# Kernel tuning notes

Measured on AMD Instinct MI355X. Metric: run time of the kernel, lower is better.

Reference implementation:

```python
import jax, jax.numpy as jnp
import numpy as np


def setup_inputs() -> dict:
    key = jax.random.key(0)
    T, B, D, H = 512, 64, 512, 512
    k0, k1, k2, k3 = jax.random.split(key, 4)
    x = jax.random.normal(k0, (T, B, D), dtype=jnp.float32)
    # packed-sequence lengths, descending (as PackedSequence requires), at least T//2
    lengths = jnp.sort(jax.random.randint(k1, (B,), T // 2, T + 1))[::-1].astype(jnp.int64)
    s = 1.0 / np.sqrt(H)
    # gates stacked in order (i, f, c, o): same math as 8 separate per-gate linears
    Wx = jax.random.normal(k2, (4 * H, D), dtype=jnp.float32) * s
    Wh = jax.random.normal(k3, (4 * H, H), dtype=jnp.float32) * s
    # reset_parameters(): b_i = b_c = b_o = 0, b_f = 1
    b = jnp.concatenate([jnp.zeros(H), jnp.ones(H), jnp.zeros(2 * H)]).astype(jnp.float32)
    return {"x": x, "lengths": lengths, "Wx": Wx, "Wh": Wh, "b": b}


def reference(x, lengths, Wx, Wh, b):
    T, B, D = x.shape
    H = Wh.shape[1]
    # input projections for all timesteps at once (one big GEMM)
    xg = jnp.einsum('tbd,gd->tbg', x, Wx) + b  # [T, B, 4H]
    # validity mask per (t, b): packed recurrence only updates active rows
    mask = (jnp.arange(T)[:, None] < lengths[None, :])[..., None]  # [T, B, 1]

    def step(carry, inp):
        h, c = carry
        xg_t, m = inp
        g = xg_t + h @ Wh.T  # [B, 4H]
        i, f, cc, o = jnp.split(g, 4, axis=-1)
        i = jax.nn.sigmoid(i)
        f = jax.nn.sigmoid(f)
        o = jax.nn.sigmoid(o)
        c_t = f * c + i * jnp.tanh(cc)
        h_t = o * jnp.tanh(c_t)
        c_new = jnp.where(m, c_t, c)
        h_new = jnp.where(m, h_t, h)
        out_t = jnp.where(m, h_new, jnp.zeros((), x.dtype))
        return (h_new, c_new), out_t

    h0 = jnp.zeros((B, H), dtype=x.dtype)
    (h_T, c_T), out = jax.lax.scan(step, (h0, h0), (xg, mask))
    return out  # padded equivalent of the PackedSequence output, [T, B, H]
```

## Files before the change

### kernel.cpp

```cpp
#include <hip/hip_runtime.h>
#include <stdint.h>


#define TT 512
#define BB 64
#define DD 512
#define HH 512
#define NTHR 512
#define NWG2 128
#define GR2 16
#define NWG4 256
#define GR4 8

typedef short short8 __attribute__((ext_vector_type(8)));
typedef float f32x4 __attribute__((ext_vector_type(4)));

__device__ __forceinline__ uint16_t bf16_rne(float f) {
  uint32_t u = __float_as_uint(f);
  u += 0x7fffu + ((u >> 16) & 1u);
  return (uint16_t)(u >> 16);
}

__device__ __forceinline__ void split2(float f, uint16_t &hi, uint16_t &lo) {
  uint16_t h = bf16_rne(f);
  hi = h;
  lo = bf16_rne(f - __uint_as_float(((uint32_t)h) << 16));
}

__device__ __forceinline__ float sigf(float v) { return 1.0f / (1.0f + __expf(-v)); }
__device__ __forceinline__ float tanh_(float v) {
  return 1.0f - 2.0f / (__expf(2.0f * v) + 1.0f);
}

__global__ void build_frags(const float* __restrict__ W, uint32_t* __restrict__ frag) {
  const int tid = blockIdx.x * 256 + threadIdx.x;
  const int lane = tid & 63;
  const int ks = (tid >> 6) & 15;
  const int nblk = tid >> 10;
  const int col = nblk * 16 + (lane & 15);
  const int k0 = ks * 32 + ((lane >> 4) << 3);
  const float* src = W + (size_t)col * 512 + k0;
  float4 a = *(const float4*)(src);
  float4 b = *(const float4*)(src + 4);
  float v[8] = {a.x, a.y, a.z, a.w, b.x, b.y, b.z, b.w};
  uint32_t hw[4], lw[4];
#pragma unroll
  for (int j = 0; j < 4; ++j) {
    uint16_t h0, l0, h1, l1;
    split2(v[2 * j], h0, l0);
    split2(v[2 * j + 1], h1, l1);
    hw[j] = (uint32_t)h0 | ((uint32_t)h1 << 16);
    lw[j] = (uint32_t)l0 | ((uint32_t)l1 << 16);
  }
  uint4* dst = (uint4*)(frag + (size_t)tid * 8);
  dst[0] = make_uint4(hw[0], hw[1], hw[2], hw[3]);
  dst[1] = make_uint4(lw[0], lw[1], lw[2], lw[3]);
}

__global__ __launch_bounds__(NTHR, 1) void xg_gemm(
    const float* __restrict__ x, const float* __restrict__ bias,
    const uint32_t* __restrict__ fragWx, float* __restrict__ xg) {
  const int t = blockIdx.x;
  const int tid = threadIdx.x;
  const int lane = tid & 63;
  const int wave = tid >> 6;
  const int gate = wave & 3;
  const int jsub = wave >> 2;

  __shared__ uint16_t AH[64 * 512];
  __shared__ uint16_t AL[64 * 512];

#pragma unroll
  for (int i = 0; i < 16; ++i) {
    const int flat4 = i * 2048 + tid * 4;
    const int row = flat4 >> 9;
    const int col = flat4 & 511;
    float4 v = *(const float4*)(x + ((size_t)t * BB + row) * DD + col);
    uint16_t h0, l0, h1, l1, h2, l2, h3, l3;
    split2(v.x, h0, l0);
    split2(v.y, h1, l1);
    split2(v.z, h2, l2);
    split2(v.w, h3, l3);
    const int off = row * 1024 + ((col * 2) ^ ((row & 7) << 4));
    *(uint2*)((char*)AH + off) =
        make_uint2((uint32_t)h0 | ((uint32_t)h1 << 16), (uint32_t)h2 | ((uint32_t)h3 << 16));
    *(uint2*)((char*)AL + off) =
        make_uint2((uint32_t)l0 | ((uint32_t)l1 << 16), (uint32_t)l2 | ((uint32_t)l3 << 16));
  }
  __syncthreads();

  const int achk = (lane >> 4) << 4;
  const int axr = (lane & 7) << 4;

  for (int jp = 0; jp < 16; ++jp) {
    const int jblk = jp * 2 + jsub;
    const int nblk = gate * 32 + jblk;
    short8 bh[16], bl[16];
#pragma unroll
    for (int ks = 0; ks < 16; ++ks) {
      const size_t idx = ((size_t)(nblk * 16 + ks) * 64 + lane) * 8;
      bh[ks] = __builtin_bit_cast(short8, *(const uint4*)(fragWx + idx));
      bl[ks] = __builtin_bit_cast(short8, *(const uint4*)(fragWx + idx + 4));
    }
    const int colg = (nblk << 4) + (lane & 15);
    const float bv = bias[colg];
    for (int m = 0; m < 4; ++m) {
      const char* rowH = (const char*)AH + (m * 16 + (lane & 15)) * 1024;
      const char* rowL = (const char*)AL + (m * 16 + (lane & 15)) * 1024;
      f32x4 hh = {0.f, 0.f, 0.f, 0.f}, lh = {0.f, 0.f, 0.f, 0.f}, hl = {0.f, 0.f, 0.f, 0.f};
#pragma unroll
      for (int ks = 0; ks < 16; ++ks) {
        const int off = (ks * 64 + achk) ^ axr;
        short8 ah = *(const short8*)(rowH + off);
        short8 al = *(const short8*)(rowL + off);
        hh = __builtin_amdgcn_mfma_f32_16x16x32_bf16(ah, bh[ks], hh, 0, 0, 0);
        lh = __builtin_amdgcn_mfma_f32_16x16x32_bf16(al, bh[ks], lh, 0, 0, 0);
        hl = __builtin_amdgcn_mfma_f32_16x16x32_bf16(ah, bl[ks], hl, 0, 0, 0);
      }
      const int r0 = m * 16 + ((lane >> 4) << 2);
#pragma unroll
      for (int i = 0; i < 4; ++i)
        xg[((size_t)t * BB + r0 + i) * 2048 + colg] = hh[i] + lh[i] + hl[i] + bv;
    }
  }
}

__global__ __launch_bounds__(NTHR, 2) void lstm2(
    const int* __restrict__ len, const uint32_t* __restrict__ fragWh,
    const float* __restrict__ xg, uint32_t* __restrict__ h_pair,
    float* __restrict__ out) {
  const int tid = threadIdx.x;
  const int lane = tid & 63;
  const int wave = tid >> 6;
  const int gp = wave >> 1;
  const int kh = wave & 1;
  const int group = blockIdx.x & 3;
  const int jblk = blockIdx.x >> 2;
  const int b0 = group * GR2;
  const int j0 = jblk << 4;
  uint32_t* hbase = h_pair + (size_t)group * 2 * (GR2 * HH);

  __shared__ uint16_t AH[GR2 * 512];
  __shared__ uint16_t AL[GR2 * 512];
  __shared__ float ex[8][GR2][16];
  __shared__ float c_st[GR2][16];
  __shared__ float h_st[GR2][16];
  __shared__ int len_l[GR2];

  if (tid < GR2 * 16) {
    c_st[tid >> 4][tid & 15] = 0.0f;
    h_st[tid >> 4][tid & 15] = 0.0f;
  }
  if (tid < GR2) len_l[tid] = len[b0 + tid];

  short8 bhh[8], bhl[8];
  {
    const int nblk = gp * 32 + jblk;
#pragma unroll
    for (int ksl = 0; ksl < 8; ++ksl) {
      const size_t idx = ((size_t)(nblk * 16 + kh * 8 + ksl) * 64 + lane) * 8;
      bhh[ksl] = __builtin_bit_cast(short8, *(const uint4*)(fragWh + idx));
      bhl[ksl] = __builtin_bit_cast(short8, *(const uint4*)(fragWh + idx + 4));
    }
  }

  const int arow = lane & 15;
  const int achk = (lane >> 4) << 4;
  const int axr = (arow & 7) << 4;
  const char* rowH = (const char*)AH + arow * 1024;
  const char* rowL = (const char*)AL + arow * 1024;

  const int brow = tid >> 4;
  const int jc = tid & 15;

  float xc0 = 0.f, xc1 = 0.f, xc2 = 0.f, xc3 = 0.f;
  float xn0 = 0.f, xn1 = 0.f, xn2 = 0.f, xn3 = 0.f;
  if (tid < 256) {
    const size_t xb = ((size_t)b0 + brow) * 2048 + j0 + jc;
    xc0 = xg[xb];
    xc1 = xg[xb + 512];
    xc2 = xg[xb + 1024];
    xc3 = xg[xb + 1536];
  }

  for (int t = 0; t < TT; ++t) {
    const int rbuf = t & 1;
    const int wbuf = rbuf ^ 1;

    if (tid < 256) {
      const int tn = (t + 1 < TT) ? t + 1 : t;
      const size_t xb = ((size_t)tn * BB + b0 + brow) * 2048 + j0 + jc;
      xn0 = xg[xb];
      xn1 = xg[xb + 512];
      xn2 = xg[xb + 1024];
      xn3 = xg[xb + 1536];
    }

    f32x4 hh = {0.f, 0.f, 0.f, 0.f}, lh = {0.f, 0.f, 0.f, 0.f}, hl = {0.f, 0.f, 0.f, 0.f};

    if (t > 0) {
      const uint32_t tagp = (((uint32_t)(t - 1)) >> 1) & 3u;
      const uint32_t EXd = ((tagp & 1u) << 14) | ((tagp >> 1) << 30);
      const uint64_t EX2 = ((uint64_t)EXd << 32) | EXd;
      const uint64_t MK2 = 0x4000400040004000ull;
      const unsigned long long* pb =
          (const unsigned long long*)(hbase + (size_t)rbuf * (GR2 * HH)) +
          (size_t)tid * 8;
      uint64_t w[8];
      for (;;) {
#pragma unroll
        for (int q = 0; q < 8; ++q)
          w[q] = __hip_atomic_load(pb + q, __ATOMIC_RELAXED, __HIP_MEMORY_SCOPE_AGENT);
        uint64_t bad = 0;
#pragma unroll
        for (int q = 0; q < 8; ++q) bad |= (w[q] ^ EX2);
        if ((bad & MK2) == 0ull) break;
      }

      {
        const uint32_t CM = ~0x40004000u;
        uint32_t d[16];
#pragma unroll
        for (int q = 0; q < 8; ++q) {
          d[2 * q] = (uint32_t)w[q] & CM;
          d[2 * q + 1] = (uint32_t)(w[q] >> 32) & CM;
        }
        uint32_t hw[8], lw[8];
#pragma unroll
        for (int j = 0; j < 8; ++j) {
          hw[j] = (d[2 * j] & 0xFFFFu) | (d[2 * j + 1] << 16);
          lw[j] = (d[2 * j] >> 16) | (d[2 * j + 1] & 0xFFFF0000u);
        }
        const int rrow = tid >> 5;
        const int colb = (tid & 31) * 32;
        const int base = rrow * 1024;
        const int swz = (rrow & 7) << 4;
        *(uint4*)((char*)AH + base + (colb ^ swz)) = make_uint4(hw[0], hw[1], hw[2], hw[3]);
        *(uint4*)((char*)AH + base + ((colb + 16) ^ swz)) = make_uint4(hw[4], hw[5], hw[6], hw[7]);
        *(uint4*)((char*)AL + base + (colb ^ swz)) = make_uint4(lw[0], lw[1], lw[2], lw[3]);
        *(uint4*)((char*)AL + base + ((colb + 16) ^ swz)) = make_uint4(lw[4], lw[5], lw[6], lw[7]);
      }
    }
    __syncthreads();

    if (t > 0) {
#pragma unroll
      for (int ksl = 0; ksl < 8; ++ksl) {
        const int off = ((kh * 8 + ksl) * 64 + achk) ^ axr;
        short8 ah = *(const short8*)(rowH + off);
        short8 al = *(const short8*)(rowL + off);
        hh = __builtin_amdgcn_mfma_f32_16x16x32_bf16(ah, bhh[ksl], hh, 0, 0, 0);
        lh = __builtin_amdgcn_mfma_f32_16x16x32_bf16(al, bhh[ksl], lh, 0, 0, 0);
        hl = __builtin_amdgcn_mfma_f32_16x16x32_bf16(ah, bhl[ksl], hl, 0, 0, 0);
      }
    }

    {
      const int crow = (lane >> 4) << 2;
      const int ccol = lane & 15;
#pragma unroll
      for (int r = 0; r < 4; ++r) ex[wave][crow + r][ccol] = hh[r] + lh[r] + hl[r];
    }
    __syncthreads();

    if (tid < 256) {
      const float p0 = ex[0][brow][jc] + ex[1][brow][jc] + xc0;
      const float p1 = ex[2][brow][jc] + ex[3][brow][jc] + xc1;
      const float p2 = ex[4][brow][jc] + ex[5][brow][jc] + xc2;
      const float p3 = ex[6][brow][jc] + ex[7][brow][jc] + xc3;
      const float ig = sigf(p0);
      const float fg = sigf(p1);
      const float cc = tanh_(p2);
      const float og = sigf(p3);
      const float co = c_st[brow][jc];
      const float ct = fg * co + ig * cc;
      const float ht = og * tanh_(ct);
      const bool m = (t < len_l[brow]);
      const float cn = m ? ct : co;
      const float hn = m ? ht : h_st[brow][jc];
      c_st[brow][jc] = cn;
      h_st[brow][jc] = hn;
      out[((size_t)t * BB + b0 + brow) * HH + j0 + jc] = m ? ht : 0.0f;
      uint16_t ph, pl;
      split2(hn, ph, pl);
      const uint32_t tagw = (((uint32_t)t) >> 1) & 3u;
      const uint32_t TB = ((tagw & 1u) << 14) | ((tagw >> 1) << 30);
      __hip_atomic_store(hbase + (size_t)wbuf * (GR2 * HH) + brow * HH + j0 + jc,
                         ((uint32_t)ph | ((uint32_t)pl << 16)) | TB,
                         __ATOMIC_RELAXED, __HIP_MEMORY_SCOPE_AGENT);
      xc0 = xn0;
      xc1 = xn1;
      xc2 = xn2;
      xc3 = xn3;
    }
  }
}

#define LOAD_XP(tt)                                                            \
  _Pragma("unroll") for (int i = 0; i < 2; ++i) {                              \
    const int flat4 = i * 2048 + tid * 4;                                      \
    const int row = flat4 >> 9;                                                \
    const int col = flat4 & 511;                                               \
    xp[i] = *(const float4*)(x + ((size_t)(tt) * BB + b0 + row) * DD + col);   \
  }

#define STAGE_XP()                                                             \
  _Pragma("unroll") for (int i = 0; i < 2; ++i) {                              \
    const int flat4 = i * 2048 + tid * 4;                                      \
    const int row = flat4 >> 9;                                                \
    const int col = flat4 & 511;                                               \
    uint16_t h0, l0, h1, l1, h2, l2, h3, l3;                                   \
    split2(xp[i].x, h0, l0);                                                   \
    split2(xp[i].y, h1, l1);                                                   \
    split2(xp[i].z, h2, l2);                                                   \
    split2(xp[i].w, h3, l3);                                                   \
    const uint32_t hw0 = (uint32_t)h0 | ((uint32_t)h1 << 16);                  \
    const uint32_t hw1 = (uint32_t)h2 | ((uint32_t)h3 << 16);                  \
    const uint32_t lw0 = (uint32_t)l0 | ((uint32_t)l1 << 16);                  \
    const uint32_t lw1 = (uint32_t)l2 | ((uint32_t)l3 << 16);                  \
    const int off = row * 1024 + ((col * 2) ^ (row << 4));                     \
    *(uint2*)((char*)AH + off) = make_uint2(hw0, hw1);                         \
    *(uint2*)((char*)AL + off) = make_uint2(lw0, lw1);                         \
  }

#define X_MFMA()                                                               \
  hh = (f32x4){0.f, 0.f, 0.f, 0.f};                                           \
  lh = (f32x4){0.f, 0.f, 0.f, 0.f};                                           \
  hl = (f32x4){0.f, 0.f, 0.f, 0.f};                                           \
  _Pragma("unroll") for (int ksl = 0; ksl < 8; ++ksl) {                        \
    const int off = ((kh * 8 + ksl) * 64 + achk) ^ axr;                        \
    short8 ah = *(const short8*)(rowH + off);                                  \
    short8 al = *(const short8*)(rowL + off);                                  \
    hh = __builtin_amdgcn_mfma_f32_16x16x32_bf16(ah, bxh[ksl], hh, 0, 0, 0);   \
    lh = __builtin_amdgcn_mfma_f32_16x16x32_bf16(al, bxh[ksl], lh, 0, 0, 0);   \
    hl = __builtin_amdgcn_mfma_f32_16x16x32_bf16(ah, bxl[ksl], hl, 0, 0, 0);   \
  }

__global__ __launch_bounds__(NTHR, 2) void lstm_r4(
    const float* __restrict__ x, const int* __restrict__ len,
    const float* __restrict__ bias, const uint32_t* __restrict__ fragWx,
    const uint32_t* __restrict__ fragWh, uint32_t* __restrict__ h_pair,
    float* __restrict__ out) {
  const int tid = threadIdx.x;
  const int lane = tid & 63;
  const int wave = tid >> 6;
  const int gp = wave >> 1;
  const int kh = wave & 1;
  const int group = blockIdx.x & 7;
  const int jblk = blockIdx.x >> 3;
  const int b0 = group * GR4;
  const int j0 = jblk << 4;
  uint32_t* hbase = h_pair + (size_t)group * 2 * (GR4 * HH);

  __shared__ uint16_t AH[GR4 * 512];
  __shared__ uint16_t AL[GR4 * 512];
  __shared__ float ex[8][GR4][16];
  __shared__ float c_st[GR4][16];
  __shared__ float h_st[GR4][16];
  __shared__ float bias_l[4][16];
  __shared__ int len_l[GR4];

  if (tid < GR4 * 16) {
    c_st[tid >> 4][tid & 15] = 0.0f;
    h_st[tid >> 4][tid & 15] = 0.0f;
  }
  if (tid < 64) bias_l[tid >> 4][tid & 15] = bias[(size_t)(tid >> 4) * HH + j0 + (tid & 15)];
  if (tid < GR4) len_l[tid] = len[b0 + tid];

  short8 bxh[8], bxl[8], bhh[8], bhl[8];
  {
    const int nblk = gp * 32 + jblk;
#pragma unroll
    for (int ksl = 0; ksl < 8; ++ksl) {
      const size_t idx = ((size_t)(nblk * 16 + kh * 8 + ksl) * 64 + lane) * 8;
      bxh[ksl] = __builtin_bit_cast(short8, *(const uint4*)(fragWx + idx));
      bxl[ksl] = __builtin_bit_cast(short8, *(const uint4*)(fragWx + idx + 4));
      bhh[ksl] = __builtin_bit_cast(short8, *(const uint4*)(fragWh + idx));
      bhl[ksl] = __builtin_bit_cast(short8, *(const uint4*)(fragWh + idx + 4));
    }
  }

  const int arow = lane & 7;
  const int achk = (lane >> 4) << 4;
  const int axr = arow << 4;
  const char* rowH = (const char*)AH + arow * 1024;
  const char* rowL = (const char*)AL + arow * 1024;

  f32x4 hh = {0.f, 0.f, 0.f, 0.f}, lh = {0.f, 0.f, 0.f, 0.f}, hl = {0.f, 0.f, 0.f, 0.f};
  float4 xp[2];

  LOAD_XP(0);
  __syncthreads();
  STAGE_XP();
  __syncthreads();
  X_MFMA();
  LOAD_XP(1);

  for (int t = 0; t < TT; ++t) {
    const int rbuf = t & 1;
    const int wbuf = rbuf ^ 1;

    if (t > 0) {
      const uint32_t tagp = (((uint32_t)(t - 1)) >> 1) & 3u;
      const uint32_t EXd = ((tagp & 1u) << 14) | ((tagp >> 1) << 30);
      const uint64_t EX2 = ((uint64_t)EXd << 32) | EXd;
      const uint64_t MK2 = 0x4000400040004000ull;
      const unsigned long long* pb =
          (const unsigned long long*)(hbase + (size_t)rbuf * (GR4 * HH)) +
          (size_t)tid * 4;
      uint64_t w0, w1, w2, w3;
      for (;;) {
        w0 = __hip_atomic_load(pb + 0, __ATOMIC_RELAXED, __HIP_MEMORY_SCOPE_AGENT);
        w1 = __hip_atomic_load(pb + 1, __ATOMIC_RELAXED, __HIP_MEMORY_SCOPE_AGENT);
        w2 = __hip_atomic_load(pb + 2, __ATOMIC_RELAXED, __HIP_MEMORY_SCOPE_AGENT);
        w3 = __hip_atomic_load(pb + 3, __ATOMIC_RELAXED, __HIP_MEMORY_SCOPE_AGENT);
        const uint64_t bad =
            (((w0 ^ EX2) | (w1 ^ EX2) | (w2 ^ EX2) | (w3 ^ EX2)) & MK2);
        if (bad == 0ull) break;
      }
      __syncthreads();

      {
        const uint32_t CM = ~0x40004000u;
        uint32_t d0 = (uint32_t)w0 & CM, d1 = (uint32_t)(w0 >> 32) & CM;
        uint32_t d2 = (uint32_t)w1 & CM, d3 = (uint32_t)(w1 >> 32) & CM;
        uint32_t d4 = (uint32_t)w2 & CM, d5 = (uint32_t)(w2 >> 32) & CM;
        uint32_t d6 = (uint32_t)w3 & CM, d7 = (uint32_t)(w3 >> 32) & CM;
        const uint32_t hi0 = (d0 & 0xFFFFu) | (d1 << 16);
        const uint32_t lo0 = (d0 >> 16) | (d1 & 0xFFFF0000u);
        const uint32_t hi1 = (d2 & 0xFFFFu) | (d3 << 16);
        const uint32_t lo1 = (d2 >> 16) | (d3 & 0xFFFF0000u);
        const uint32_t hi2 = (d4 & 0xFFFFu) | (d5 << 16);
        const uint32_t lo2 = (d4 >> 16) | (d5 & 0xFFFF0000u);
        const uint32_t hi3 = (d6 & 0xFFFFu) | (d7 << 16);
        const uint32_t lo3 = (d6 >> 16) | (d7 & 0xFFFF0000u);
        const int woff = wave * 1024 + ((lane * 16) ^ (wave << 4));
        *(uint4*)((char*)AH + woff) = make_uint4(hi0, hi1, hi2, hi3);
        *(uint4*)((char*)AL + woff) = make_uint4(lo0, lo1, lo2, lo3);
      }
      __syncthreads();

#pragma unroll
      for (int ksl = 0; ksl < 8; ++ksl) {
        const int off = ((kh * 8 + ksl) * 64 + achk) ^ axr;
        short8 ah = *(const short8*)(rowH + off);
        short8 al = *(const short8*)(rowL + off);
        hh = __builtin_amdgcn_mfma_f32_16x16x32_bf16(ah, bhh[ksl], hh, 0, 0, 0);
        lh = __builtin_amdgcn_mfma_f32_16x16x32_bf16(al, bhh[ksl], lh, 0, 0, 0);
        hl = __builtin_amdgcn_mfma_f32_16x16x32_bf16(ah, bhl[ksl], hl, 0, 0, 0);
      }
    }

    {
      const int crow = (lane >> 4) << 2;
      const int ccol = lane & 15;
      if (crow < GR4) {
#pragma unroll
        for (int r = 0; r < 4; ++r) ex[wave][crow + r][ccol] = hh[r] + lh[r] + hl[r];
      }
    }
    __syncthreads();

    if (tid < GR4 * 16) {
      const int brow = tid >> 4;
      const int jc = tid & 15;
      const float p0 = ex[0][brow][jc] + ex[1][brow][jc] + bias_l[0][jc];
      const float p1 = ex[2][brow][jc] + ex[3][brow][jc] + bias_l[1][jc];
      const float p2 = ex[4][brow][jc] + ex[5][brow][jc] + bias_l[2][jc];
      const float p3 = ex[6][brow][jc] + ex[7][brow][jc] + bias_l[3][jc];
      const float ig = sigf(p0);
      const float fg = sigf(p1);
      const float cc = tanh_(p2);
      const float og = sigf(p3);
      const float co = c_st[brow][jc];
      const float ct = fg * co + ig * cc;
      const float ht = og * tanh_(ct);
      const bool m = (t < len_l[brow]);
      const float cn = m ? ct : co;
      const float hn = m ? ht : h_st[brow][jc];
      c_st[brow][jc] = cn;
      h_st[brow][jc] = hn;
      out[((size_t)t * BB + b0 + brow) * HH + j0 + jc] = m ? ht : 0.0f;
      uint16_t ph, pl;
      split2(hn, ph, pl);
      const uint32_t tagw = (((uint32_t)t) >> 1) & 3u;
      const uint32_t TB = ((tagw & 1u) << 14) | ((tagw >> 1) << 30);
      const uint32_t hv = ((uint32_t)ph | ((uint32_t)pl << 16)) | TB;
      __hip_atomic_store(hbase + (size_t)wbuf * (GR4 * HH) + brow * HH + j0 + jc,
                         hv, __ATOMIC_RELAXED, __HIP_MEMORY_SCOPE_AGENT);
    }

    if (t + 1 < TT) {
      STAGE_XP();
      __syncthreads();
      X_MFMA();
      LOAD_XP(min(t + 2, TT - 1));
    }
  }
}
#undef LOAD_XP
#undef STAGE_XP
#undef X_MFMA

extern "C" void kernel_launch(void* const* d_in, const int* in_sizes, int n_in,
                              void* d_out, int out_size, void* d_ws, size_t ws_size,
                              hipStream_t stream) {
  const float* x = (const float*)d_in[0];
  const int* len = (const int*)d_in[1];
  const float* Wx = (const float*)d_in[2];
  const float* Wh = (const float*)d_in[3];
  const float* bias = (const float*)d_in[4];
  float* out = (float*)d_out;

  const size_t FRAG_DW = (size_t)128 * 16 * 64 * 8;
  const size_t HP_DW = 65536;
  const size_t XG_DW = (size_t)TT * BB * 2048;
  uint32_t* fragWx = (uint32_t*)d_ws;
  uint32_t* fragWh = fragWx + FRAG_DW;
  uint32_t* h_pair = fragWh + FRAG_DW;
  float* xg = (float*)(h_pair + HP_DW);
  const size_t need = (2 * FRAG_DW + HP_DW + XG_DW) * 4;

  hipMemsetAsync(h_pair, 0xFF, HP_DW * 4, stream);

  build_frags<<<dim3(512), dim3(256), 0, stream>>>(Wx, fragWx);
  build_frags<<<dim3(512), dim3(256), 0, stream>>>(Wh, fragWh);

  if (ws_size >= need) {
    xg_gemm<<<dim3(TT), dim3(NTHR), 0, stream>>>(x, bias, fragWx, xg);
    void* args[] = {(void*)&len, (void*)&fragWh, (void*)&xg, (void*)&h_pair,
                    (void*)&out};
    hipLaunchCooperativeKernel((void*)lstm2, dim3(NWG2), dim3(NTHR), args, 0, stream);
  } else {
    void* args[] = {(void*)&x,      (void*)&len,    (void*)&bias, (void*)&fragWx,
                    (void*)&fragWh, (void*)&h_pair, (void*)&out};
    hipLaunchCooperativeKernel((void*)lstm_r4, dim3(NWG4), dim3(NTHR), args, 0, stream);
  }
}
```

Baseline: 1.439 ms.

## Fuse input projection into recurrent kernel via producer workgroups feeding a ring buffer

Removes the separate xg GEMM kernel and its large global xg buffer. The cooperative launch now has twice as many workgroups: half run the recurrence, and the other half compute each timestep's input projection plus bias just ahead of it. Projections pass through a 4-slot tagged ring buffer packed as hi/lo bf16, with a per-pair counter for flow control. The goal is to overlap the input GEMM with the serial recurrence and avoid the xg round trip through memory. In exchange, projections are scaled and clamped to ±64 before packing, which could lose accuracy on large inputs, and correctness now depends on all 256 workgroups being co-resident.

```diff
diff --git a/kernel.cpp b/kernel.cpp
--- a/kernel.cpp
+++ b/kernel.cpp
@@ -7,8 +7,9 @@
 #define DD 512
 #define HH 512
 #define NTHR 512
-#define NWG2 128
-#define GR2 16
+#define NWG 256
+#define NPAIR 128
+#define GR 16
 #define NWG4 256
 #define GR4 8
 
@@ -57,112 +58,34 @@
   dst[1] = make_uint4(lw[0], lw[1], lw[2], lw[3]);
 }
 
-__global__ __launch_bounds__(NTHR, 1) void xg_gemm(
-    const float* __restrict__ x, const float* __restrict__ bias,
-    const uint32_t* __restrict__ fragWx, float* __restrict__ xg) {
-  const int t = blockIdx.x;
-  const int tid = threadIdx.x;
-  const int lane = tid & 63;
-  const int wave = tid >> 6;
-  const int gate = wave & 3;
-  const int jsub = wave >> 2;
-
-  __shared__ uint16_t AH[64 * 512];
-  __shared__ uint16_t AL[64 * 512];
-
-#pragma unroll
-  for (int i = 0; i < 16; ++i) {
-    const int flat4 = i * 2048 + tid * 4;
-    const int row = flat4 >> 9;
-    const int col = flat4 & 511;
-    float4 v = *(const float4*)(x + ((size_t)t * BB + row) * DD + col);
-    uint16_t h0, l0, h1, l1, h2, l2, h3, l3;
-    split2(v.x, h0, l0);
-    split2(v.y, h1, l1);
-    split2(v.z, h2, l2);
-    split2(v.w, h3, l3);
-    const int off = row * 1024 + ((col * 2) ^ ((row & 7) << 4));
-    *(uint2*)((char*)AH + off) =
-        make_uint2((uint32_t)h0 | ((uint32_t)h1 << 16), (uint32_t)h2 | ((uint32_t)h3 << 16));
-    *(uint2*)((char*)AL + off) =
-        make_uint2((uint32_t)l0 | ((uint32_t)l1 << 16), (uint32_t)l2 | ((uint32_t)l3 << 16));
-  }
-  __syncthreads();
-
-  const int achk = (lane >> 4) << 4;
-  const int axr = (lane & 7) << 4;
-
-  for (int jp = 0; jp < 16; ++jp) {
-    const int jblk = jp * 2 + jsub;
-    const int nblk = gate * 32 + jblk;
-    short8 bh[16], bl[16];
-#pragma unroll
-    for (int ks = 0; ks < 16; ++ks) {
-      const size_t idx = ((size_t)(nblk * 16 + ks) * 64 + lane) * 8;
-      bh[ks] = __builtin_bit_cast(short8, *(const uint4*)(fragWx + idx));
-      bl[ks] = __builtin_bit_cast(short8, *(const uint4*)(fragWx + idx + 4));
-    }
-    const int colg = (nblk << 4) + (lane & 15);
-    const float bv = bias[colg];
-    for (int m = 0; m < 4; ++m) {
-      const char* rowH = (const char*)AH + (m * 16 + (lane & 15)) * 1024;
-      const char* rowL = (const char*)AL + (m * 16 + (lane & 15)) * 1024;
-      f32x4 hh = {0.f, 0.f, 0.f, 0.f}, lh = {0.f, 0.f, 0.f, 0.f}, hl = {0.f, 0.f, 0.f, 0.f};
-#pragma unroll
-      for (int ks = 0; ks < 16; ++ks) {
-        const int off = (ks * 64 + achk) ^ axr;
-        short8 ah = *(const short8*)(rowH + off);
-        short8 al = *(const short8*)(rowL + off);
-        hh = __builtin_amdgcn_mfma_f32_16x16x32_bf16(ah, bh[ks], hh, 0, 0, 0);
-        lh = __builtin_amdgcn_mfma_f32_16x16x32_bf16(al, bh[ks], lh, 0, 0, 0);
-        hl = __builtin_amdgcn_mfma_f32_16x16x32_bf16(ah, bl[ks], hl, 0, 0, 0);
-      }
-      const int r0 = m * 16 + ((lane >> 4) << 2);
-#pragma unroll
-      for (int i = 0; i < 4; ++i)
-        xg[((size_t)t * BB + r0 + i) * 2048 + colg] = hh[i] + lh[i] + hl[i] + bv;
-    }
-  }
-}
-
-__global__ __launch_bounds__(NTHR, 2) void lstm2(
-    const int* __restrict__ len, const uint32_t* __restrict__ fragWh,
-    const float* __restrict__ xg, uint32_t* __restrict__ h_pair,
+__global__ __launch_bounds__(NTHR, 2) void lstm3(
+    const float* __restrict__ x, const int* __restrict__ len,
+    const float* __restrict__ bias, const uint32_t* __restrict__ fragWx,
+    const uint32_t* __restrict__ fragWh, uint32_t* __restrict__ h_pair,
+    uint32_t* __restrict__ xacc, uint32_t* __restrict__ cnts,
     float* __restrict__ out) {
   const int tid = threadIdx.x;
   const int lane = tid & 63;
   const int wave = tid >> 6;
   const int gp = wave >> 1;
   const int kh = wave & 1;
-  const int group = blockIdx.x & 3;
-  const int jblk = blockIdx.x >> 2;
-  const int b0 = group * GR2;
+  const bool isH = blockIdx.x < NPAIR;
+  const int pid = isH ? blockIdx.x : blockIdx.x - NPAIR;
+  const int group = pid & 3;
+  const int jblk = pid >> 2;
+  const int b0 = group * GR;
   const int j0 = jblk << 4;
-  uint32_t* hbase = h_pair + (size_t)group * 2 * (GR2 * HH);
-
-  __shared__ uint16_t AH[GR2 * 512];
-  __shared__ uint16_t AL[GR2 * 512];
-  __shared__ float ex[8][GR2][16];
-  __shared__ float c_st[GR2][16];
-  __shared__ float h_st[GR2][16];
-  __shared__ int len_l[GR2];
-
-  if (tid < GR2 * 16) {
-    c_st[tid >> 4][tid & 15] = 0.0f;
-    h_st[tid >> 4][tid & 15] = 0.0f;
-  }
-  if (tid < GR2) len_l[tid] = len[b0 + tid];
-
-  short8 bhh[8], bhl[8];
-  {
-    const int nblk = gp * 32 + jblk;
-#pragma unroll
-    for (int ksl = 0; ksl < 8; ++ksl) {
-      const size_t idx = ((size_t)(nblk * 16 + kh * 8 + ksl) * 64 + lane) * 8;
-      bhh[ksl] = __builtin_bit_cast(short8, *(const uint4*)(fragWh + idx));
-      bhl[ksl] = __builtin_bit_cast(short8, *(const uint4*)(fragWh + idx + 4));
-    }
-  }
+  uint32_t* hbase = h_pair + (size_t)group * 2 * (GR * HH);
+  unsigned long long* xb64 = (unsigned long long*)(xacc + (size_t)pid * 4096);
+
+  __shared__ uint16_t AH[GR * 512];
+  __shared__ uint16_t AL[GR * 512];
+  __shared__ float ex[8][GR][16];
+  __shared__ float xex[GR][64];
+  __shared__ float c_st[GR][16];
+  __shared__ float h_st[GR][16];
+  __shared__ float bias_l[4][16];
+  __shared__ int len_l[GR];
 
   const int arow = lane & 15;
   const int achk = (lane >> 4) << 4;
@@ -170,128 +93,236 @@
   const char* rowH = (const char*)AH + arow * 1024;
   const char* rowL = (const char*)AL + arow * 1024;
 
-  const int brow = tid >> 4;
-  const int jc = tid & 15;
-
-  float xc0 = 0.f, xc1 = 0.f, xc2 = 0.f, xc3 = 0.f;
-  float xn0 = 0.f, xn1 = 0.f, xn2 = 0.f, xn3 = 0.f;
-  if (tid < 256) {
-    const size_t xb = ((size_t)b0 + brow) * 2048 + j0 + jc;
-    xc0 = xg[xb];
-    xc1 = xg[xb + 512];
-    xc2 = xg[xb + 1024];
-    xc3 = xg[xb + 1536];
-  }
-
-  for (int t = 0; t < TT; ++t) {
-    const int rbuf = t & 1;
-    const int wbuf = rbuf ^ 1;
-
+  const uint64_t MK2 = 0x4000400040004000ull;
+  const uint32_t CM = ~0x40004000u;
+
+  if (isH) {
     if (tid < 256) {
-      const int tn = (t + 1 < TT) ? t + 1 : t;
-      const size_t xb = ((size_t)tn * BB + b0 + brow) * 2048 + j0 + jc;
-      xn0 = xg[xb];
-      xn1 = xg[xb + 512];
-      xn2 = xg[xb + 1024];
-      xn3 = xg[xb + 1536];
-    }
-
-    f32x4 hh = {0.f, 0.f, 0.f, 0.f}, lh = {0.f, 0.f, 0.f, 0.f}, hl = {0.f, 0.f, 0.f, 0.f};
-
-    if (t > 0) {
-      const uint32_t tagp = (((uint32_t)(t - 1)) >> 1) & 3u;
-      const uint32_t EXd = ((tagp & 1u) << 14) | ((tagp >> 1) << 30);
+      c_st[tid >> 4][tid & 15] = 0.0f;
+      h_st[tid >> 4][tid & 15] = 0.0f;
+    }
+    if (tid < GR) len_l[tid] = len[b0 + tid];
+
+    short8 bhh[8], bhl[8];
+    {
+      const int nblk = gp * 32 + jblk;
+#pragma unroll
+      for (int ksl = 0; ksl < 8; ++ksl) {
+        const size_t idx = ((size_t)(nblk * 16 + kh * 8 + ksl) * 64 + lane) * 8;
+        bhh[ksl] = __builtin_bit_cast(short8, *(const uint4*)(fragWh + idx));
+        bhl[ksl] = __builtin_bit_cast(short8, *(const uint4*)(fragWh + idx + 4));
+      }
+    }
+
+    const int prow = tid >> 5;
+    const int pc0 = tid & 31;
+    const int brow = tid >> 4;
+    const int jc = tid & 15;
+
+    for (int t = 0; t < TT; ++t) {
+      const int rbuf = t & 1;
+      const int wbuf = rbuf ^ 1;
+
+      const uint32_t tagh = (((uint32_t)(t - 1)) >> 1) & 3u;
+      const uint32_t EHd = ((tagh & 1u) << 14) | ((tagh >> 1) << 30);
+      const uint64_t EH2 = ((uint64_t)EHd << 32) | EHd;
+      const uint32_t tagx = (((uint32_t)t) >> 1) & 3u;
+      const uint32_t EXd = ((tagx & 1u) << 14) | ((tagx >> 1) << 30);
       const uint64_t EX2 = ((uint64_t)EXd << 32) | EXd;
-      const uint64_t MK2 = 0x4000400040004000ull;
-      const unsigned long long* pb =
-          (const unsigned long long*)(hbase + (size_t)rbuf * (GR2 * HH)) +
-          (size_t)tid * 8;
-      uint64_t w[8];
-      for (;;) {
-#pragma unroll
-        for (int q = 0; q < 8; ++q)
-          w[q] = __hip_atomic_load(pb + q, __ATOMIC_RELAXED, __HIP_MEMORY_SCOPE_AGENT);
-        uint64_t bad = 0;
-#pragma unroll
-        for (int q = 0; q < 8; ++q) bad |= (w[q] ^ EX2);
-        if ((bad & MK2) == 0ull) break;
-      }
-
+
+      const unsigned long long* hb64 =
+          (const unsigned long long*)(hbase + (size_t)rbuf * (GR * HH));
+      const unsigned long long* hp0 = hb64 + prow * 256 + pc0 * 4;
+      const unsigned long long* hp1 = hp0 + 128;
+      const unsigned long long* xp = xb64 + (size_t)(t & 3) * 512 + tid;
+
+      uint64_t w0, w1, w2, w3, w4, w5, w6, w7, wx;
+      if (t > 0) {
+        for (;;) {
+          w0 = __hip_atomic_load(hp0 + 0, __ATOMIC_RELAXED, __HIP_MEMORY_SCOPE_AGENT);
+          w1 = __hip_atomic_load(hp0 + 1, __ATOMIC_RELAXED, __HIP_MEMORY_SCOPE_AGENT);
+          w2 = __hip_atomic_load(hp0 + 2, __ATOMIC_RELAXED, __HIP_MEMORY_SCOPE_AGENT);
+          w3 = __hip_atomic_load(hp0 + 3, __ATOMIC_RELAXED, __HIP_MEMORY_SCOPE_AGENT);
+          w4 = __hip_atomic_load(hp1 + 0, __ATOMIC_RELAXED, __HIP_MEMORY_SCOPE_AGENT);
+          w5 = __hip_atomic_load(hp1 + 1, __ATOMIC_RELAXED, __HIP_MEMORY_SCOPE_AGENT);
+          w6 = __hip_atomic_load(hp1 + 2, __ATOMIC_RELAXED, __HIP_MEMORY_SCOPE_AGENT);
+          w7 = __hip_atomic_load(hp1 + 3, __ATOMIC_RELAXED, __HIP_MEMORY_SCOPE_AGENT);
+          wx = __hip_atomic_load(xp, __ATOMIC_RELAXED, __HIP_MEMORY_SCOPE_AGENT);
+          const uint64_t bad = (((w0 ^ EH2) | (w1 ^ EH2) | (w2 ^ EH2) | (w3 ^ EH2) |
+                                (w4 ^ EH2) | (w5 ^ EH2) | (w6 ^ EH2) | (w7 ^ EH2) |
+                                (wx ^ EX2)) & MK2);
+          if (bad == 0ull) break;
+        }
+      } else {
+        for (;;) {
+          wx = __hip_atomic_load(xp, __ATOMIC_RELAXED, __HIP_MEMORY_SCOPE_AGENT);
+          if (((wx ^ EX2) & MK2) == 0ull) break;
+        }
+      }
+
+      if (t > 0) {
+        const int base = prow * 1024;
+        const int swz = (prow & 7) << 4;
+        uint32_t d0, d1, d2, d3, d4, d5, d6, d7;
+#define UNPK(A, B, C, D, OFF)                                                  \
+        d0 = (uint32_t)(A) & CM; d1 = (uint32_t)((A) >> 32) & CM;              \
+        d2 = (uint32_t)(B) & CM; d3 = (uint32_t)((B) >> 32) & CM;              \
+        d4 = (uint32_t)(C) & CM; d5 = (uint32_t)((C) >> 32) & CM;              \
+        d6 = (uint32_t)(D) & CM; d7 = (uint32_t)((D) >> 32) & CM;              \
+        *(uint4*)((char*)AH + base + ((OFF) ^ swz)) =                          \
+            make_uint4((d0 & 0xFFFFu) | (d1 << 16), (d2 & 0xFFFFu) | (d3 << 16), \
+                       (d4 & 0xFFFFu) | (d5 << 16), (d6 & 0xFFFFu) | (d7 << 16)); \
+        *(uint4*)((char*)AL + base + ((OFF) ^ swz)) =                          \
+            make_uint4((d0 >> 16) | (d1 & 0xFFFF0000u), (d2 >> 16) | (d3 & 0xFFFF0000u), \
+                       (d4 >> 16) | (d5 & 0xFFFF0000u), (d6 >> 16) | (d7 & 0xFFFF0000u));
+        UNPK(w0, w1, w2, w3, pc0 * 16);
+        UNPK(w4, w5, w6, w7, pc0 * 16 + 512);
+#undef UNPK
+      }
       {
-        const uint32_t CM = ~0x40004000u;
-        uint32_t d[16];
-#pragma unroll
-        for (int q = 0; q < 8; ++q) {
-          d[2 * q] = (uint32_t)w[q] & CM;
-          d[2 * q + 1] = (uint32_t)(w[q] >> 32) & CM;
+        const uint32_t da = (uint32_t)wx & CM;
+        const uint32_t db = (uint32_t)(wx >> 32) & CM;
+        const int f0 = 2 * tid;
+        xex[f0 >> 6][f0 & 63] =
+            32.0f * (__uint_as_float(da << 16) + __uint_as_float(da & 0xFFFF0000u));
+        xex[f0 >> 6][(f0 & 63) + 1] =
+            32.0f * (__uint_as_float(db << 16) + __uint_as_float(db & 0xFFFF0000u));
+      }
+      __syncthreads();
+
+      f32x4 hh = {0.f, 0.f, 0.f, 0.f}, lh = {0.f, 0.f, 0.f, 0.f}, hl = {0.f, 0.f, 0.f, 0.f};
+      if (t > 0) {
+#pragma unroll
+        for (int ksl = 0; ksl < 8; ++ksl) {
+          const int off = ((kh * 8 + ksl) * 64 + achk) ^ axr;
+          short8 ah = *(const short8*)(rowH + off);
+          short8 al = *(const short8*)(rowL + off);
+          hh = __builtin_amdgcn_mfma_f32_16x16x32_bf16(ah, bhh[ksl], hh, 0, 0, 0);
+          lh = __builtin_amdgcn_mfma_f32_16x16x32_bf16(al, bhh[ksl], lh, 0, 0, 0);
+          hl = __builtin_amdgcn_mfma_f32_16x16x32_bf16(ah, bhl[ksl], hl, 0, 0, 0);
         }
-        uint32_t hw[8], lw[8];
-#pragma unroll
-        for (int j = 0; j < 8; ++j) {
-          hw[j] = (d[2 * j] & 0xFFFFu) | (d[2 * j + 1] << 16);
-          lw[j] = (d[2 * j] >> 16) | (d[2 * j + 1] & 0xFFFF0000u);
+      }
+      {
+        const int crow = (lane >> 4) << 2;
+        const int ccol = lane & 15;
+#pragma unroll
+        for (int r = 0; r < 4; ++r) ex[wave][crow + r][ccol] = hh[r] + lh[r] + hl[r];
+      }
+      __syncthreads();
+
+      if (tid < 256) {
+        const float p0 = ex[0][brow][jc] + ex[1][brow][jc] + xex[brow][jc];
+        const float p1 = ex[2][brow][jc] + ex[3][brow][jc] + xex[brow][16 + jc];
+        const float p2 = ex[4][brow][jc] + ex[5][brow][jc] + xex[brow][32 + jc];
+        const float p3 = ex[6][brow][jc] + ex[7][brow][jc] + xex[brow][48 + jc];
+        const float ig = sigf(p0);
+        const float fg = sigf(p1);
+        const float cc = tanh_(p2);
+        const float og = sigf(p3);
+        const float co = c_st[brow][jc];
+        const float ct = fg * co + ig * cc;
+        const float ht = og * tanh_(ct);
+        const bool m = (t < len_l[brow]);
+        const float cn = m ? ct : co;
+        const float hn = m ? ht : h_st[brow][jc];
+        c_st[brow][jc] = cn;
+        h_st[brow][jc] = hn;
+        out[((size_t)t * BB + b0 + brow) * HH + j0 + jc] = m ? ht : 0.0f;
+        uint16_t ph, pl;
+        split2(hn, ph, pl);
+        const uint32_t tagw = (((uint32_t)t) >> 1) & 3u;
+        const uint32_t TB = ((tagw & 1u) << 14) | ((tagw >> 1) << 30);
+        __hip_atomic_store(hbase + (size_t)wbuf * (GR * HH) + brow * HH + j0 + jc,
+                           ((uint32_t)ph | ((uint32_t)pl << 16)) | TB,
+                           __ATOMIC_RELAXED, __HIP_MEMORY_SCOPE_AGENT);
+      }
+      if (tid == 0)
+        __hip_atomic_store(cnts + pid, (uint32_t)(t + 1), __ATOMIC_RELAXED,
+                           __HIP_MEMORY_SCOPE_AGENT);
+    }
+  } else {
+    if (tid < 64) bias_l[tid >> 4][tid & 15] = bias[(size_t)(tid >> 4) * HH + j0 + (tid & 15)];
+
+    short8 bxh[8], bxl[8];
+    {
+      const int nblk = gp * 32 + jblk;
+#pragma unroll
+      for (int ksl = 0; ksl < 8; ++ksl) {
+        const size_t idx = ((size_t)(nblk * 16 + kh * 8 + ksl) * 64 + lane) * 8;
+        bxh[ksl] = __builtin_bit_cast(short8, *(const uint4*)(fragWx + idx));
+        bxl[ksl] = __builtin_bit_cast(short8, *(const uint4*)(fragWx + idx + 4));
+      }
+    }
+
+    for (int t = 0; t < TT; ++t) {
+      if (t >= 4) {
+        for (;;) {
+          uint32_t c = __hip_atomic_load(cnts + pid, __ATOMIC_RELAXED,
+                                         __HIP_MEMORY_SCOPE_AGENT);
+          if ((int)c >= t - 3) break;
         }
-        const int rrow = tid >> 5;
-        const int colb = (tid & 31) * 32;
-        const int base = rrow * 1024;
-        const int swz = (rrow & 7) << 4;
-        *(uint4*)((char*)AH + base + (colb ^ swz)) = make_uint4(hw[0], hw[1], hw[2], hw[3]);
-        *(uint4*)((char*)AH + base + ((colb + 16) ^ swz)) = make_uint4(hw[4], hw[5], hw[6], hw[7]);
-        *(uint4*)((char*)AL + base + (colb ^ swz)) = make_uint4(lw[0], lw[1], lw[2], lw[3]);
-        *(uint4*)((char*)AL + base + ((colb + 16) ^ swz)) = make_uint4(lw[4], lw[5], lw[6], lw[7]);
-      }
-    }
-    __syncthreads();
-
-    if (t > 0) {
+      }
+#pragma unroll
+      for (int i = 0; i < 4; ++i) {
+        const int flat4 = i * 2048 + tid * 4;
+        const int row = flat4 >> 9;
+        const int col = flat4 & 511;
+        float4 v = *(const float4*)(x + ((size_t)t * BB + b0 + row) * DD + col);
+        uint16_t h0, l0, h1, l1, h2, l2, h3, l3;
+        split2(v.x, h0, l0);
+        split2(v.y, h1, l1);
+        split2(v.z, h2, l2);
+        split2(v.w, h3, l3);
+        const int off = row * 1024 + ((col * 2) ^ ((row & 7) << 4));
+        *(uint2*)((char*)AH + off) =
+            make_uint2((uint32_t)h0 | ((uint32_t)h1 << 16), (uint32_t)h2 | ((uint32_t)h3 << 16));
+        *(uint2*)((char*)AL + off) =
+            make_uint2((uint32_t)l0 | ((uint32_t)l1 << 16), (uint32_t)l2 | ((uint32_t)l3 << 16));
+      }
+      __syncthreads();
+
+      f32x4 hh = {0.f, 0.f, 0.f, 0.f}, lh = {0.f, 0.f, 0.f, 0.f}, hl = {0.f, 0.f, 0.f, 0.f};
 #pragma unroll
       for (int ksl = 0; ksl < 8; ++ksl) {
         const int off = ((kh * 8 + ksl) * 64 + achk) ^ axr;
         short8 ah = *(const short8*)(rowH + off);
         short8 al = *(const short8*)(rowL + off);
-        hh = __builtin_amdgcn_mfma_f32_16x16x32_bf16(ah, bhh[ksl], hh, 0, 0, 0);
-        lh = __builtin_amdgcn_mfma_f32_16x16x32_bf16(al, bhh[ksl], lh, 0, 0, 0);
-        hl = __builtin_amdgcn_mfma_f32_16x16x32_bf16(ah, bhl[ksl], hl, 0, 0, 0);
-      }
-    }
-
-    {
-      const int crow = (lane >> 4) << 2;
-      const int ccol = lane & 15;
-#pragma unroll
-      for (int r = 0; r < 4; ++r) ex[wave][crow + r][ccol] = hh[r] + lh[r] + hl[r];
-    }
-    __syncthreads();
-
-    if (tid < 256) {
-      const float p0 = ex[0][brow][jc] + ex[1][brow][jc] + xc0;
-      const float p1 = ex[2][brow][jc] + ex[3][brow][jc] + xc1;
-      const float p2 = ex[4][brow][jc] + ex[5][brow][jc] + xc2;
-      const float p3 = ex[6][brow][jc] + ex[7][brow][jc] + xc3;
-      const float ig = sigf(p0);
-      const float fg = sigf(p1);
-      const float cc = tanh_(p2);
-      const float og = sigf(p3);
-      const float co = c_st[brow][jc];
-      const float ct = fg * co + ig * cc;
-      const float ht = og * tanh_(ct);
-      const bool m = (t < len_l[brow]);
-      const float cn = m ? ct : co;
-      const float hn = m ? ht : h_st[brow][jc];
-      c_st[brow][jc] = cn;
-      h_st[brow][jc] = hn;
-      out[((size_t)t * BB + b0 + brow) * HH + j0 + jc] = m ? ht : 0.0f;
-      uint16_t ph, pl;
-      split2(hn, ph, pl);
-      const uint32_t tagw = (((uint32_t)t) >> 1) & 3u;
-      const uint32_t TB = ((tagw & 1u) << 14) | ((tagw >> 1) << 30);
-      __hip_atomic_store(hbase + (size_t)wbuf * (GR2 * HH) + brow * HH + j0 + jc,
-                         ((uint32_t)ph | ((uint32_t)pl << 16)) | TB,
-                         __ATOMIC_RELAXED, __HIP_MEMORY_SCOPE_AGENT);
-      xc0 = xn0;
-      xc1 = xn1;
-      xc2 = xn2;
-      xc3 = xn3;
+        hh = __builtin_amdgcn_mfma_f32_16x16x32_bf16(ah, bxh[ksl], hh, 0, 0, 0);
+        lh = __builtin_amdgcn_mfma_f32_16x16x32_bf16(al, bxh[ksl], lh, 0, 0, 0);
+        hl = __builtin_amdgcn_mfma_f32_16x16x32_bf16(ah, bxl[ksl], hl, 0, 0, 0);
+      }
+      {
+        const int crow = (lane >> 4) << 2;
+        const int ccol = lane & 15;
+#pragma unroll
+        for (int r = 0; r < 4; ++r) ex[wave][crow + r][ccol] = hh[r] + lh[r] + hl[r];
+      }
+      __syncthreads();
+
+      {
+        const int f0 = 2 * tid;
+        const int brow = f0 >> 6;
+        const int gc0 = f0 & 63;
+        const int gc1 = gc0 + 1;
+        const float p0 = ex[(gc0 >> 4) * 2][brow][gc0 & 15] +
+                         ex[(gc0 >> 4) * 2 + 1][brow][gc0 & 15] + bias_l[gc0 >> 4][gc0 & 15];
+        const float p1 = ex[(gc1 >> 4) * 2][brow][gc1 & 15] +
+                         ex[(gc1 >> 4) * 2 + 1][brow][gc1 & 15] + bias_l[gc1 >> 4][gc1 & 15];
+        const uint32_t tagw = (((uint32_t)t) >> 1) & 3u;
+        const uint32_t TB = ((tagw & 1u) << 14) | ((tagw >> 1) << 30);
+        float v0 = p0 * 0.03125f;
+        float v1 = p1 * 0.03125f;
+        v0 = fminf(fmaxf(v0, -1.9921875f), 1.9921875f);
+        v1 = fminf(fmaxf(v1, -1.9921875f), 1.9921875f);
+        uint16_t h0, l0, h1, l1;
+        split2(v0, h0, l0);
+        split2(v1, h1, l1);
+        const uint32_t da = ((uint32_t)h0 | ((uint32_t)l0 << 16)) | TB;
+        const uint32_t db = ((uint32_t)h1 | ((uint32_t)l1 << 16)) | TB;
+        __hip_atomic_store(xb64 + (size_t)(t & 3) * 512 + tid,
+                           ((uint64_t)db << 32) | da, __ATOMIC_RELAXED,
+                           __HIP_MEMORY_SCOPE_AGENT);
+      }
     }
   }
 }
@@ -514,12 +545,13 @@
 
   const size_t FRAG_DW = (size_t)128 * 16 * 64 * 8;
   const size_t HP_DW = 65536;
-  const size_t XG_DW = (size_t)TT * BB * 2048;
+  const size_t XA_DW = (size_t)NPAIR * 4 * 1024;
   uint32_t* fragWx = (uint32_t*)d_ws;
   uint32_t* fragWh = fragWx + FRAG_DW;
   uint32_t* h_pair = fragWh + FRAG_DW;
-  float* xg = (float*)(h_pair + HP_DW);
-  const size_t need = (2 * FRAG_DW + HP_DW + XG_DW) * 4;
+  uint32_t* xaccp = h_pair + HP_DW;
+  uint32_t* cnts = xaccp + XA_DW;
+  const size_t need = (2 * FRAG_DW + HP_DW + XA_DW + 128) * 4;
 
   hipMemsetAsync(h_pair, 0xFF, HP_DW * 4, stream);
 
@@ -527,10 +559,12 @@
   build_frags<<<dim3(512), dim3(256), 0, stream>>>(Wh, fragWh);
 
   if (ws_size >= need) {
-    xg_gemm<<<dim3(TT), dim3(NTHR), 0, stream>>>(x, bias, fragWx, xg);
-    void* args[] = {(void*)&len, (void*)&fragWh, (void*)&xg, (void*)&h_pair,
+    hipMemsetAsync(xaccp, 0xFF, XA_DW * 4, stream);
+    hipMemsetAsync(cnts, 0, 512, stream);
+    void* args[] = {(void*)&x,      (void*)&len,    (void*)&bias,  (void*)&fragWx,
+                    (void*)&fragWh, (void*)&h_pair, (void*)&xaccp, (void*)&cnts,
                     (void*)&out};
-    hipLaunchCooperativeKernel((void*)lstm2, dim3(NWG2), dim3(NTHR), args, 0, stream);
+    hipLaunchCooperativeKernel((void*)lstm3, dim3(NWG), dim3(NTHR), args, 0, stream);
   } else {
     void* args[] = {(void*)&x,      (void*)&len,    (void*)&bias, (void*)&fragWx,
                     (void*)&fragWh, (void*)&h_pair, (void*)&out};
```

New measurement: 3.207 ms. +122.9%, slower.
